# Optimization experiments

Measured on AMD Instinct MI355X. Metric: run time of the kernel, lower is better.

Reference implementation:

```python
import jax, jax.numpy as jnp
import numpy as np

COMMITMENT_COST = 0.25
NUM_EMBEDDINGS = 1024
EMBEDDING_DIM = 64


def setup_inputs() -> dict:
    key = jax.random.key(0)
    k1, k2 = jax.random.split(key)
    x = jax.random.normal(k1, (32, 64, 64, 64), dtype=jnp.float32)
    embeddings = jax.random.normal(k2, (EMBEDDING_DIM, NUM_EMBEDDINGS), dtype=jnp.float32)
    return {"x": x, "embeddings": embeddings}


def reference(x, embeddings):
    # x: [..., D], embeddings: [D, K]
    flat = jnp.reshape(x, (-1, EMBEDDING_DIM))                       # [N, D]
    # squared euclidean distances via ||a||^2 - 2 a.e + ||e||^2      # [N, K]
    distances = (jnp.sum(flat * flat, axis=1, keepdims=True)
                 - 2.0 * (flat @ embeddings)
                 + jnp.sum(embeddings * embeddings, axis=0, keepdims=True))
    flat_indices = jnp.argmax(-distances, axis=1)                    # [N]
    encodings = jax.nn.one_hot(flat_indices, NUM_EMBEDDINGS, dtype=distances.dtype)  # [N, K]
    encoding_indices = jnp.reshape(flat_indices, x.shape[:-1])
    # gather codebook rows: embeddings.T[idx]
    quantized = jnp.take(embeddings.T, encoding_indices, axis=0)     # same shape as x
    e_latent_loss = jnp.mean((jax.lax.stop_gradient(quantized) - x) ** 2)
    q_latent_loss = jnp.mean((quantized - jax.lax.stop_gradient(x)) ** 2)
    loss = q_latent_loss + COMMITMENT_COST * e_latent_loss
    quantized_st = x + jax.lax.stop_gradient(quantized - x)          # straight-through
    avg_probs = jnp.mean(encodings, axis=0)                          # [K]
    perplexity = jnp.exp(-jnp.sum(avg_probs * jnp.log(avg_probs + 1e-10)))
    return quantized_st, loss, perplexity, encodings, encoding_indices, distances
```

## Files before the change

kernel.cpp:

```cpp
#include <hip/hip_runtime.h>
#include <hip/hip_bf16.h>
#include <math.h>

#define NROWS 131072
#define DDIM  64
#define KCODE 1024
#define TAU_B 0.008f

#define OFF_Q    0L
#define OFF_LOSS 8388608L
#define OFF_PERP 8388609L
#define OFF_ENC  8388610L
#define OFF_IDX  (OFF_ENC + 134217728L)
#define OFF_DIST (OFF_IDX + 131072L)

#define WS_ENORM 0L
#define WS_ET    1024L
#define WS_EBPH  66560L
#define WS_EBPL  99328L
#define WS_CNT   263168L
#define WS_PART  395268L

typedef short bf16x8 __attribute__((ext_vector_type(8)));
typedef float f32x4  __attribute__((ext_vector_type(4)));
typedef float f32x2  __attribute__((ext_vector_type(2)));

__device__ inline unsigned short f2bf(float f) {
    unsigned u = __float_as_uint(f);
    unsigned r = (u + 0x7fffu + ((u >> 16) & 1u)) >> 16;
    return (unsigned short)r;
}
__device__ inline float bf2f(unsigned short h) {
    return __uint_as_float(((unsigned)h) << 16);
}
__device__ inline int dswz(int i) { return i ^ (((i >> 12) & 3) << 3); }

__global__ __launch_bounds__(256) void k1a_prep(const float* __restrict__ e,
                                                float* __restrict__ enorm,
                                                float* __restrict__ eT,
                                                int* __restrict__ cnt) {
    int k = blockIdx.x * 256 + threadIdx.x;
    float s = 0.f;
    #pragma unroll 8
    for (int d = 0; d < DDIM; ++d) {
        float v = e[(size_t)d * KCODE + k];
        s = fmaf(v, v, s);
        eT[(size_t)k * DDIM + d] = v;
    }
    enorm[k] = s;
    cnt[k] = 0;
}

__global__ __launch_bounds__(128) void k1b_pack(const float* __restrict__ e,
                                                unsigned short* __restrict__ ebph,
                                                unsigned short* __restrict__ ebpl) {
    const int gct = blockIdx.x;
    const int ks  = threadIdx.x >> 6;
    const int l   = threadIdx.x & 63;
    const int col = (gct << 4) | (l & 15);
    const int kb  = (ks << 5) + ((l >> 4) << 3);
    const size_t ob = ((size_t)((gct << 1) | ks) * 64 + l) * 8;
    #pragma unroll
    for (int j = 0; j < 8; ++j) {
        float f = e[(size_t)(kb + j) * KCODE + col];
        unsigned short h = f2bf(f);
        float lo = f - bf2f(h);
        ebph[ob + j] = h;
        ebpl[ob + j] = f2bf(lo);
    }
}

__global__ __launch_bounds__(256) void kA_fused(const float* __restrict__ x,
                                                const float* __restrict__ e,
                                                const unsigned short* __restrict__ ebph,
                                                const unsigned short* __restrict__ ebpl,
                                                const float* __restrict__ enorm,
                                                const float* __restrict__ eT,
                                                float* __restrict__ dist,
                                                float* __restrict__ enc,
                                                float* __restrict__ outq,
                                                float* __restrict__ outidx,
                                                int* __restrict__ cnt,
                                                float* __restrict__ partials) {
    __shared__ __align__(16) float dt[16384];
    __shared__ float hd[2];
    __shared__ short xh[16 * 64];
    __shared__ short xl[16 * 64];
    __shared__ float pn[16][16];
    __shared__ float xn[16];
    __shared__ float enl[KCODE];
    __shared__ float wm1[4][16], wm2[4][16];
    __shared__ int   wi1[4][16];
    __shared__ float ps[16];
    __shared__ int   sidx[16];
    __shared__ int   nearmask;
    __shared__ float xsh[DDIM];
    __shared__ double wbv[4];
    __shared__ int    wbi[4];

    const int tid  = threadIdx.x;
    const int lane = tid & 63;
    const int w    = tid >> 6;
    const int rowbase = blockIdx.x * 16;

    {
        if (tid == 0) nearmask = 0;
        float4 v = ((const float4*)(x + (size_t)rowbase * DDIM))[tid];
        int fi = tid * 4, r = fi >> 6, c = fi & 63;
        float fv[4] = {v.x, v.y, v.z, v.w};
        short hv[4], lv[4];
        #pragma unroll
        for (int q = 0; q < 4; ++q) {
            unsigned short hh = f2bf(fv[q]);
            hv[q] = (short)hh;
            lv[q] = (short)f2bf(fv[q] - bf2f(hh));
        }
        *(short4*)&xh[r * 64 + c] = make_short4(hv[0], hv[1], hv[2], hv[3]);
        *(short4*)&xl[r * 64 + c] = make_short4(lv[0], lv[1], lv[2], lv[3]);
        pn[r][c >> 2] = fmaf(v.x, v.x, fmaf(v.y, v.y, fmaf(v.z, v.z, v.w * v.w)));
        ((float4*)enl)[tid] = ((const float4*)enorm)[tid];
    }
    __syncthreads();
    if (tid < 16) {
        float s = 0.f;
        #pragma unroll
        for (int j = 0; j < 16; ++j) s += pn[tid][j];
        xn[tid] = s;
    }
    __syncthreads();

    const int arow = lane & 15, akb = (lane >> 4) << 3;
    bf16x8 ah0 = *(const bf16x8*)&xh[arow * 64 + akb];
    bf16x8 ah1 = *(const bf16x8*)&xh[arow * 64 + 32 + akb];
    bf16x8 al0 = *(const bf16x8*)&xl[arow * 64 + akb];
    bf16x8 al1 = *(const bf16x8*)&xl[arow * 64 + 32 + akb];

    const int wr   = (lane >> 4) << 2;
    const int colb = (w << 8) | (lane & 15);
    float xnv[4];
    #pragma unroll
    for (int r = 0; r < 4; ++r) xnv[r] = xn[wr + r];
    float env[16];
    #pragma unroll
    for (int ct = 0; ct < 16; ++ct) env[ct] = enl[colb + (ct << 4)];

    float m1[4], m2[4];
    int   i1[4];
    #pragma unroll
    for (int r = 0; r < 4; ++r) { m1[r] = 3.4e38f; m2[r] = 3.4e38f; i1[r] = 1 << 30; }

    #pragma unroll 4
    for (int ct = 0; ct < 16; ++ct) {
        const int gct = (w << 4) | ct;
        const size_t bo = ((size_t)(gct << 1) * 64 + lane) * 8;
        bf16x8 bh0 = *(const bf16x8*)(ebph + bo);
        bf16x8 bh1 = *(const bf16x8*)(ebph + bo + 512);
        bf16x8 bl0 = *(const bf16x8*)(ebpl + bo);
        bf16x8 bl1 = *(const bf16x8*)(ebpl + bo + 512);

        f32x4 d = {0.f, 0.f, 0.f, 0.f};
        d = __builtin_amdgcn_mfma_f32_16x16x32_bf16(ah0, bh0, d, 0, 0, 0);
        d = __builtin_amdgcn_mfma_f32_16x16x32_bf16(ah1, bh1, d, 0, 0, 0);
        d = __builtin_amdgcn_mfma_f32_16x16x32_bf16(ah0, bl0, d, 0, 0, 0);
        d = __builtin_amdgcn_mfma_f32_16x16x32_bf16(ah1, bl1, d, 0, 0, 0);
        d = __builtin_amdgcn_mfma_f32_16x16x32_bf16(al0, bh0, d, 0, 0, 0);
        d = __builtin_amdgcn_mfma_f32_16x16x32_bf16(al1, bh1, d, 0, 0, 0);

        const int col = colb + (ct << 4);
        #pragma unroll
        for (int r = 0; r < 4; ++r) {
            float o = fmaf(-2.f, d[r], xnv[r] + env[ct]);
            if (o < m1[r]) { m2[r] = m1[r]; m1[r] = o; i1[r] = col; }
            else if (o < m2[r]) m2[r] = o;
            const int fl = ((wr + r) << 10) + col;
            if (fl >= 2) dt[dswz(fl - 2)] = o;
            else         hd[fl] = o;
        }
    }

    #pragma unroll
    for (int m = 1; m < 16; m <<= 1) {
        #pragma unroll
        for (int r = 0; r < 4; ++r) {
            float om1 = __shfl_xor(m1[r], m);
            int   oi1 = __shfl_xor(i1[r], m);
            float om2 = __shfl_xor(m2[r], m);
            if (om1 < m1[r] || (om1 == m1[r] && oi1 < i1[r])) {
                m2[r] = fminf(m1[r], om2); m1[r] = om1; i1[r] = oi1;
            } else {
                m2[r] = fminf(m2[r], om1);
            }
        }
    }
    if ((lane & 15) == 0) {
        #pragma unroll
        for (int r = 0; r < 4; ++r) {
            wm1[w][wr + r] = m1[r];
            wm2[w][wr + r] = m2[r];
            wi1[w][wr + r] = i1[r];
        }
    }
    __syncthreads();
    if (tid < 16) {
        float bm1 = wm1[0][tid], bm2 = wm2[0][tid];
        int   bi  = wi1[0][tid];
        #pragma unroll
        for (int wv = 1; wv < 4; ++wv) {
            float om1 = wm1[wv][tid], om2 = wm2[wv][tid];
            int   oi  = wi1[wv][tid];
            if (om1 < bm1 || (om1 == bm1 && oi < bi)) {
                bm2 = fminf(bm1, om2); bm1 = om1; bi = oi;
            } else {
                bm2 = fminf(bm2, om1);
            }
        }
        sidx[tid] = bi;
        ps[tid]   = bm1;
        if (bm2 - bm1 < TAU_B) atomicOr(&nearmask, 1 << tid);
    }
    __syncthreads();

    {
        float* dbase = dist + ((size_t)rowbase << 10);
        #pragma unroll
        for (int j = 0; j < 16; ++j) {
            const int s = (j << 8) + tid;
            if (s < 4095) {
                const int i0 = s << 2;
                f32x4 v = *(const f32x4*)&dt[dswz(i0)];
                *(f32x4*)(dbase + 2 + i0) = v;
            }
        }
        if (tid == 255) {
            const int it = dswz(16380);
            *(f32x2*)(dbase)         = (f32x2){hd[0], hd[1]};
            *(f32x2*)(dbase + 16382) = (f32x2){dt[it], dt[it + 1]};
        }
    }

    if (nearmask) {
        for (int mrow = nearmask; mrow; mrow &= (mrow - 1)) {
            const int r = __ffs(mrow) - 1;
            if (tid < DDIM) xsh[tid] = x[(size_t)(rowbase + r) * DDIM + tid];
            __syncthreads();
            const int k0 = tid * 4;
            double dd[4] = {0.0, 0.0, 0.0, 0.0};
            for (int d = 0; d < DDIM; ++d) {
                double xd = (double)xsh[d];
                float4 ev = *(const float4*)(e + (size_t)d * KCODE + k0);
                double t0 = xd - (double)ev.x; dd[0] = fma(t0, t0, dd[0]);
                double t1 = xd - (double)ev.y; dd[1] = fma(t1, t1, dd[1]);
                double t2 = xd - (double)ev.z; dd[2] = fma(t2, t2, dd[2]);
                double t3 = xd - (double)ev.w; dd[3] = fma(t3, t3, dd[3]);
            }
            double best = dd[0]; int bidx = k0;
            #pragma unroll
            for (int c = 1; c < 4; ++c)
                if (dd[c] < best) { best = dd[c]; bidx = k0 + c; }
            #pragma unroll
            for (int m = 1; m < 64; m <<= 1) {
                double ob = __shfl_xor(best, m);
                int    oi = __shfl_xor(bidx, m);
                if (ob < best || (ob == best && oi < bidx)) { best = ob; bidx = oi; }
            }
            if (lane == 0) { wbv[w] = best; wbi[w] = bidx; }
            __syncthreads();
            if (tid == 0) {
                double bb = wbv[0]; int bi = wbi[0];
                #pragma unroll
                for (int wv = 1; wv < 4; ++wv)
                    if (wbv[wv] < bb || (wbv[wv] == bb && wbi[wv] < bi)) {
                        bb = wbv[wv]; bi = wbi[wv];
                    }
                sidx[r] = bi; ps[r] = (float)bb;
            }
            __syncthreads();
        }
    }

    if (tid < 16) {
        const int idx = sidx[tid];
        outidx[rowbase + tid] = (float)idx;
        atomicAdd(cnt + idx, 1);
    }
    {
        const int r = tid >> 4, c = tid & 15;
        const int idx = sidx[r];
        f32x4 ev = *(const f32x4*)(eT + (size_t)idx * DDIM + (c << 2));
        *((f32x4*)(outq + ((size_t)(rowbase + r) << 6)) + c) = ev;
    }
    {
        float* ebase = enc + ((size_t)rowbase << 10);
        #pragma unroll
        for (int j = 0; j < 16; ++j) {
            const int s = (j << 8) + tid;
            if (s < 4095) {
                const int fb = 2 + (s << 2);
                const int r0 = fb >> 10, c0 = fb & 1023;
                const int i0 = sidx[r0];
                f32x4 v;
                if (c0 != 1022) {
                    v.x = (c0     == i0) ? 1.f : 0.f;
                    v.y = (c0 + 1 == i0) ? 1.f : 0.f;
                    v.z = (c0 + 2 == i0) ? 1.f : 0.f;
                    v.w = (c0 + 3 == i0) ? 1.f : 0.f;
                } else {
                    const int i1b = sidx[r0 + 1];
                    v.x = (1022 == i0)  ? 1.f : 0.f;
                    v.y = (1023 == i0)  ? 1.f : 0.f;
                    v.z = (0    == i1b) ? 1.f : 0.f;
                    v.w = (1    == i1b) ? 1.f : 0.f;
                }
                *(f32x4*)(ebase + fb) = v;
            }
        }
        if (tid == 255) {
            f32x2 h, t;
            h.x = (0 == sidx[0]) ? 1.f : 0.f;
            h.y = (1 == sidx[0]) ? 1.f : 0.f;
            t.x = (1022 == sidx[15]) ? 1.f : 0.f;
            t.y = (1023 == sidx[15]) ? 1.f : 0.f;
            *(f32x2*)(ebase) = h;
            *(f32x2*)(ebase + 16382) = t;
        }
    }
    __syncthreads();
    if (tid == 0) {
        float s = 0.f;
        #pragma unroll
        for (int j = 0; j < 16; ++j) s += ps[j];
        partials[blockIdx.x] = s;
    }
}

__global__ __launch_bounds__(256) void k6_scalar(const float* __restrict__ partials,
                                                 const int* __restrict__ cnt,
                                                 float* __restrict__ outloss,
                                                 float* __restrict__ outperp) {
    __shared__ double sd[256];
    const int tid = threadIdx.x;
    double s = 0.0;
    for (int i = tid; i < 8192; i += 256) s += (double)partials[i];
    sd[tid] = s;
    __syncthreads();
    for (int st = 128; st > 0; st >>= 1) {
        if (tid < st) sd[tid] += sd[tid + st];
        __syncthreads();
    }
    const double total = sd[0];
    __syncthreads();
    double h = 0.0;
    for (int k = tid; k < KCODE; k += 256) {
        double p = (double)cnt[k] / (double)NROWS;
        h -= p * log(p + 1e-10);
    }
    sd[tid] = h;
    __syncthreads();
    for (int st = 128; st > 0; st >>= 1) {
        if (tid < st) sd[tid] += sd[tid + st];
        __syncthreads();
    }
    if (tid == 0) {
        *outloss = (float)(total * 1.25 / (double)((long)NROWS * DDIM));
        *outperp = (float)exp(sd[0]);
    }
}

extern "C" void kernel_launch(void* const* d_in, const int* in_sizes, int n_in,
                              void* d_out, int out_size, void* d_ws, size_t ws_size,
                              hipStream_t stream) {
    const float* x = (const float*)d_in[0];
    const float* e = (const float*)d_in[1];
    float* out = (float*)d_out;

    float* ws_f = (float*)d_ws;
    float* enorm   = ws_f + WS_ENORM;
    float* eT      = ws_f + WS_ET;
    unsigned short* ebph = (unsigned short*)(ws_f + WS_EBPH);
    unsigned short* ebpl = (unsigned short*)(ws_f + WS_EBPL);
    int*   cnt     = (int*)(ws_f + WS_CNT);
    float* partials= ws_f + WS_PART;

    float* outq    = out + OFF_Q;
    float* outloss = out + OFF_LOSS;
    float* outperp = out + OFF_PERP;
    float* enc     = out + OFF_ENC;
    float* outidx  = out + OFF_IDX;
    float* dist    = out + OFF_DIST;

    hipLaunchKernelGGL(k1a_prep, dim3(4),    dim3(256), 0, stream, e, enorm, eT, cnt);
    hipLaunchKernelGGL(k1b_pack, dim3(64),   dim3(128), 0, stream, e, ebph, ebpl);
    hipLaunchKernelGGL(kA_fused, dim3(8192), dim3(256), 0, stream, x, e, ebph, ebpl, enorm,
                       eT, dist, enc, outq, outidx, cnt, partials);
    hipLaunchKernelGGL(k6_scalar,dim3(1),    dim3(256), 0, stream, partials, cnt, outloss, outperp);
}
```

Baseline: 345.1 us.

## Split fused VQ kernel and stage distances in fp16 shared memory

```diff
diff --git a/kernel.cpp b/kernel.cpp
--- a/kernel.cpp
+++ b/kernel.cpp
@@ -18,12 +18,14 @@
 #define WS_ET    1024L
 #define WS_EBPH  66560L
 #define WS_EBPL  99328L
+#define WS_IDX   132096L
 #define WS_CNT   263168L
 #define WS_PART  395268L
 
 typedef short bf16x8 __attribute__((ext_vector_type(8)));
 typedef float f32x4  __attribute__((ext_vector_type(4)));
 typedef float f32x2  __attribute__((ext_vector_type(2)));
+typedef _Float16 f16x4v __attribute__((ext_vector_type(4)));
 
 __device__ inline unsigned short f2bf(float f) {
     unsigned u = __float_as_uint(f);
@@ -33,7 +35,7 @@
 __device__ inline float bf2f(unsigned short h) {
     return __uint_as_float(((unsigned)h) << 16);
 }
-__device__ inline int dswz(int i) { return i ^ (((i >> 12) & 3) << 3); }
+__device__ inline int dswz16(int i) { return i ^ (((i >> 12) & 3) << 3); }
 
 __global__ __launch_bounds__(256) void k1a_prep(const float* __restrict__ e,
                                                 float* __restrict__ enorm,
@@ -70,25 +72,20 @@
     }
 }
 
-__global__ __launch_bounds__(256) void kA_fused(const float* __restrict__ x,
-                                                const float* __restrict__ e,
-                                                const unsigned short* __restrict__ ebph,
-                                                const unsigned short* __restrict__ ebpl,
-                                                const float* __restrict__ enorm,
-                                                const float* __restrict__ eT,
-                                                float* __restrict__ dist,
-                                                float* __restrict__ enc,
-                                                float* __restrict__ outq,
-                                                float* __restrict__ outidx,
-                                                int* __restrict__ cnt,
-                                                float* __restrict__ partials) {
-    __shared__ __align__(16) float dt[16384];
+__global__ __launch_bounds__(256, 4) void kA_dist(const float* __restrict__ x,
+                                                  const float* __restrict__ e,
+                                                  const unsigned short* __restrict__ ebph,
+                                                  const unsigned short* __restrict__ ebpl,
+                                                  const float* __restrict__ enorm,
+                                                  float* __restrict__ dist,
+                                                  int* __restrict__ idxarr,
+                                                  int* __restrict__ cnt,
+                                                  float* __restrict__ partials) {
+    __shared__ __align__(16) _Float16 dtH[16384];
     __shared__ float hd[2];
     __shared__ short xh[16 * 64];
     __shared__ short xl[16 * 64];
-    __shared__ float pn[16][16];
     __shared__ float xn[16];
-    __shared__ float enl[KCODE];
     __shared__ float wm1[4][16], wm2[4][16];
     __shared__ int   wi1[4][16];
     __shared__ float ps[16];
@@ -117,15 +114,10 @@
         }
         *(short4*)&xh[r * 64 + c] = make_short4(hv[0], hv[1], hv[2], hv[3]);
         *(short4*)&xl[r * 64 + c] = make_short4(lv[0], lv[1], lv[2], lv[3]);
-        pn[r][c >> 2] = fmaf(v.x, v.x, fmaf(v.y, v.y, fmaf(v.z, v.z, v.w * v.w)));
-        ((float4*)enl)[tid] = ((const float4*)enorm)[tid];
-    }
-    __syncthreads();
-    if (tid < 16) {
-        float s = 0.f;
-        #pragma unroll
-        for (int j = 0; j < 16; ++j) s += pn[tid][j];
-        xn[tid] = s;
+        float s4 = fmaf(v.x, v.x, fmaf(v.y, v.y, fmaf(v.z, v.z, v.w * v.w)));
+        #pragma unroll
+        for (int m = 1; m < 16; m <<= 1) s4 += __shfl_xor(s4, m);
+        if ((lane & 15) == 0) xn[r] = s4;
     }
     __syncthreads();
 
@@ -142,7 +134,7 @@
     for (int r = 0; r < 4; ++r) xnv[r] = xn[wr + r];
     float env[16];
     #pragma unroll
-    for (int ct = 0; ct < 16; ++ct) env[ct] = enl[colb + (ct << 4)];
+    for (int ct = 0; ct < 16; ++ct) env[ct] = enorm[colb + (ct << 4)];
 
     float m1[4], m2[4];
     int   i1[4];
@@ -173,7 +165,7 @@
             if (o < m1[r]) { m2[r] = m1[r]; m1[r] = o; i1[r] = col; }
             else if (o < m2[r]) m2[r] = o;
             const int fl = ((wr + r) << 10) + col;
-            if (fl >= 2) dt[dswz(fl - 2)] = o;
+            if (fl >= 2) dtH[dswz16(fl - 2)] = (_Float16)o;
             else         hd[fl] = o;
         }
     }
@@ -227,14 +219,16 @@
             const int s = (j << 8) + tid;
             if (s < 4095) {
                 const int i0 = s << 2;
-                f32x4 v = *(const f32x4*)&dt[dswz(i0)];
+                const int iw = dswz16(i0);
+                f16x4v h = *(const f16x4v*)&dtH[iw];
+                f32x4 v = {(float)h[0], (float)h[1], (float)h[2], (float)h[3]};
                 *(f32x4*)(dbase + 2 + i0) = v;
             }
         }
         if (tid == 255) {
-            const int it = dswz(16380);
+            const int it = dswz16(16380);
             *(f32x2*)(dbase)         = (f32x2){hd[0], hd[1]};
-            *(f32x2*)(dbase + 16382) = (f32x2){dt[it], dt[it + 1]};
+            *(f32x2*)(dbase + 16382) = (f32x2){(float)dtH[it], (float)dtH[it + 1]};
         }
     }
 
@@ -280,56 +274,75 @@
 
     if (tid < 16) {
         const int idx = sidx[tid];
-        outidx[rowbase + tid] = (float)idx;
+        idxarr[rowbase + tid] = idx;
         atomicAdd(cnt + idx, 1);
     }
-    {
-        const int r = tid >> 4, c = tid & 15;
-        const int idx = sidx[r];
-        f32x4 ev = *(const f32x4*)(eT + (size_t)idx * DDIM + (c << 2));
-        *((f32x4*)(outq + ((size_t)(rowbase + r) << 6)) + c) = ev;
-    }
-    {
-        float* ebase = enc + ((size_t)rowbase << 10);
-        #pragma unroll
-        for (int j = 0; j < 16; ++j) {
-            const int s = (j << 8) + tid;
-            if (s < 4095) {
-                const int fb = 2 + (s << 2);
-                const int r0 = fb >> 10, c0 = fb & 1023;
-                const int i0 = sidx[r0];
-                f32x4 v;
-                if (c0 != 1022) {
-                    v.x = (c0     == i0) ? 1.f : 0.f;
-                    v.y = (c0 + 1 == i0) ? 1.f : 0.f;
-                    v.z = (c0 + 2 == i0) ? 1.f : 0.f;
-                    v.w = (c0 + 3 == i0) ? 1.f : 0.f;
-                } else {
-                    const int i1b = sidx[r0 + 1];
-                    v.x = (1022 == i0)  ? 1.f : 0.f;
-                    v.y = (1023 == i0)  ? 1.f : 0.f;
-                    v.z = (0    == i1b) ? 1.f : 0.f;
-                    v.w = (1    == i1b) ? 1.f : 0.f;
-                }
-                *(f32x4*)(ebase + fb) = v;
-            }
-        }
-        if (tid == 255) {
-            f32x2 h, t;
-            h.x = (0 == sidx[0]) ? 1.f : 0.f;
-            h.y = (1 == sidx[0]) ? 1.f : 0.f;
-            t.x = (1022 == sidx[15]) ? 1.f : 0.f;
-            t.y = (1023 == sidx[15]) ? 1.f : 0.f;
-            *(f32x2*)(ebase) = h;
-            *(f32x2*)(ebase + 16382) = t;
-        }
-    }
-    __syncthreads();
-    if (tid == 0) {
+    if (tid == 64) {
         float s = 0.f;
         #pragma unroll
         for (int j = 0; j < 16; ++j) s += ps[j];
         partials[blockIdx.x] = s;
+    }
+}
+
+__global__ __launch_bounds__(256) void kC_final(const float* __restrict__ eT,
+                                                const int* __restrict__ idxarr,
+                                                float* __restrict__ outq,
+                                                float* __restrict__ enc,
+                                                float* __restrict__ outidx) {
+    __shared__ int sidx[64];
+    const int tid = threadIdx.x;
+    const int rowbase = blockIdx.x * 64;
+
+    if (tid < 64) {
+        const int grow = rowbase + tid;
+        const int idx = idxarr[grow];
+        sidx[tid] = idx;
+        outidx[grow] = (float)idx;
+    }
+    __syncthreads();
+
+    #pragma unroll
+    for (int it = 0; it < 4; ++it) {
+        const int row = (it << 4) + (tid >> 4);
+        const int grow = rowbase + row;
+        const int idx = sidx[row];
+        f32x4 ev = *(const f32x4*)(eT + (size_t)idx * DDIM + ((tid & 15) << 2));
+        *((f32x4*)(outq + ((size_t)grow << 6)) + (tid & 15)) = ev;
+    }
+
+    float* ebase = enc + ((size_t)rowbase << 10);
+    #pragma unroll 8
+    for (int j = 0; j < 64; ++j) {
+        const int s = (j << 8) + tid;
+        if (s < 16383) {
+            const int fb = 2 + (s << 2);
+            const int r0 = fb >> 10, c0 = fb & 1023;
+            const int i0 = sidx[r0];
+            f32x4 v;
+            if (c0 != 1022) {
+                v.x = (c0     == i0) ? 1.f : 0.f;
+                v.y = (c0 + 1 == i0) ? 1.f : 0.f;
+                v.z = (c0 + 2 == i0) ? 1.f : 0.f;
+                v.w = (c0 + 3 == i0) ? 1.f : 0.f;
+            } else {
+                const int i1b = sidx[r0 + 1];
+                v.x = (1022 == i0)  ? 1.f : 0.f;
+                v.y = (1023 == i0)  ? 1.f : 0.f;
+                v.z = (0    == i1b) ? 1.f : 0.f;
+                v.w = (1    == i1b) ? 1.f : 0.f;
+            }
+            *(f32x4*)(ebase + fb) = v;
+        }
+    }
+    if (tid == 255) {
+        f32x2 h, t;
+        h.x = (0 == sidx[0]) ? 1.f : 0.f;
+        h.y = (1 == sidx[0]) ? 1.f : 0.f;
+        t.x = (1022 == sidx[63]) ? 1.f : 0.f;
+        t.y = (1023 == sidx[63]) ? 1.f : 0.f;
+        *(f32x2*)(ebase) = h;
+        *(f32x2*)(ebase + 65534) = t;
     }
 }
 
@@ -378,6 +391,7 @@
     float* eT      = ws_f + WS_ET;
     unsigned short* ebph = (unsigned short*)(ws_f + WS_EBPH);
     unsigned short* ebpl = (unsigned short*)(ws_f + WS_EBPL);
+    int*   idxarr  = (int*)(ws_f + WS_IDX);
     int*   cnt     = (int*)(ws_f + WS_CNT);
     float* partials= ws_f + WS_PART;
 
@@ -390,7 +404,8 @@
 
     hipLaunchKernelGGL(k1a_prep, dim3(4),    dim3(256), 0, stream, e, enorm, eT, cnt);
     hipLaunchKernelGGL(k1b_pack, dim3(64),   dim3(128), 0, stream, e, ebph, ebpl);
-    hipLaunchKernelGGL(kA_fused, dim3(8192), dim3(256), 0, stream, x, e, ebph, ebpl, enorm,
-                       eT, dist, enc, outq, outidx, cnt, partials);
+    hipLaunchKernelGGL(kA_dist,  dim3(8192), dim3(256), 0, stream, x, e, ebph, ebpl, enorm,
+                       dist, idxarr, cnt, partials);
+    hipLaunchKernelGGL(kC_final, dim3(2048), dim3(256), 0, stream, eT, idxarr, outq, enc, outidx);
     hipLaunchKernelGGL(k6_scalar,dim3(1),    dim3(256), 0, stream, partials, cnt, outloss, outperp);
 }
```

Measured after the change: 339.9 us. No clear change (-1.5%).
